# Performance work log

Hardware: AMD Instinct MI355X
Metric: run time of the kernel (lower is better)

The kernel has to match this reference:

```python
import jax, jax.numpy as jnp
import numpy as np

TOPK = 10
NUM_CLASSES = 80
ALPHA = 0.5
BETA = 6.0
EPS = 1e-9
IOU_EPS = 1e-7


def _make_anchors(img=640, strides=(8, 16, 32)):
    pts = []
    for s in strides:
        n = img // s
        ax = (np.arange(n, dtype=np.float32) + 0.5) * s
        gy, gx = np.meshgrid(ax, ax, indexing='ij')
        pts.append(np.stack([gx.ravel(), gy.ravel()], axis=-1))
    return jnp.asarray(np.concatenate(pts, axis=0), dtype=jnp.float32)  # [8400, 2]


def setup_inputs() -> dict:
    key = jax.random.key(0)
    ks = jax.random.split(key, 8)
    bs, ng, nc = 32, 64, NUM_CLASSES
    anc_points = _make_anchors()
    na = anc_points.shape[0]  # 8400
    pd_scores = jax.random.uniform(ks[0], (bs, na, nc), dtype=jnp.float32)
    pwh = jax.random.uniform(ks[1], (bs, na, 2), minval=10.0, maxval=100.0)
    pxy = anc_points[None] + jax.random.normal(ks[2], (bs, na, 2)) * 8.0
    pd_bboxes = jnp.concatenate([pxy - pwh / 2, pxy + pwh / 2], axis=-1)
    gxy = jax.random.uniform(ks[3], (bs, ng, 2), minval=50.0, maxval=590.0)
    gwh = jax.random.uniform(ks[4], (bs, ng, 2), minval=20.0, maxval=200.0)
    gt_bboxes = jnp.clip(jnp.concatenate([gxy - gwh / 2, gxy + gwh / 2], axis=-1), 0.0, 640.0)
    gt_labels = jax.random.randint(ks[5], (bs, ng, 1), 0, nc)
    num_gt = jax.random.randint(ks[6], (bs,), 1, ng + 1)
    mask_gt = (jnp.arange(ng)[None, :] < num_gt[:, None])[..., None]  # bool [bs, ng, 1]
    return {"pd_scores": pd_scores, "pd_bboxes": pd_bboxes, "anc_points": anc_points,
            "gt_labels": gt_labels, "gt_bboxes": gt_bboxes, "mask_gt": mask_gt}


def _iou_xyxy(b1, b2):
    # b1: [bs, na, 1, 4], b2: [bs, 1, ng, 4] -> [bs, na, ng]
    inter_w = jnp.maximum(jnp.minimum(b1[..., 2], b2[..., 2]) - jnp.maximum(b1[..., 0], b2[..., 0]), 0.0)
    inter_h = jnp.maximum(jnp.minimum(b1[..., 3], b2[..., 3]) - jnp.maximum(b1[..., 1], b2[..., 1]), 0.0)
    inter = inter_w * inter_h
    a1 = (b1[..., 2] - b1[..., 0]) * (b1[..., 3] - b1[..., 1])
    a2 = (b2[..., 2] - b2[..., 0]) * (b2[..., 3] - b2[..., 1])
    return inter / (a1 + a2 - inter + IOU_EPS)


def _assign(pd_scores, pd_bboxes, anc_points, gt_labels, gt_bboxes, mask_gt):
    bs, na, nc = pd_scores.shape
    ng = gt_bboxes.shape[1]
    dt = pd_scores.dtype

    # --- candidates whose center lies strictly inside the GT box ---
    lt = gt_bboxes[:, None, :, :2]          # [bs,1,ng,2]
    rb = gt_bboxes[:, None, :, 2:]
    xy = anc_points[None, :, None, :]       # [1,na,1,2]
    deltas = jnp.concatenate([xy - lt, rb - xy], axis=-1)  # [bs,na,ng,4]
    mask_in_gts = deltas.min(axis=-1) > EPS                 # [bs,na,ng]
    valid = mask_gt[..., 0].astype(bool)                    # [bs,ng]
    mask = mask_in_gts & valid[:, None, :]

    # --- alignment metric = score[label]^alpha * iou^beta, zeroed outside mask ---
    labels = gt_labels[..., 0].astype(jnp.int32)            # [bs,ng]
    idx = jnp.broadcast_to(labels[:, None, :], (bs, na, ng))
    gathered = jnp.take_along_axis(pd_scores, idx, axis=2)  # [bs,na,ng]
    bbox_scores = jnp.where(mask, gathered, 0.0)
    overlaps = jnp.where(mask, _iou_xyxy(pd_bboxes[:, :, None, :], gt_bboxes[:, None, :, :]), 0.0)
    safe_scores = jnp.where(mask, gathered, 1.0)  # avoids 0**0.5 grad issues; masked out below
    align_metric = jnp.where(mask, safe_scores ** ALPHA * overlaps ** BETA, 0.0)

    # --- top-k anchors per GT (over anchor dim) ---
    k = min(TOPK, na)
    _, topk_idx = jax.lax.top_k(jnp.swapaxes(align_metric, 1, 2), k)  # [bs,ng,k]
    bidx = jnp.arange(bs)[:, None, None]
    gidx = jnp.arange(ng)[None, :, None]
    in_topk = jnp.zeros((bs, ng, na), dtype=bool).at[bidx, gidx, topk_idx].set(True)
    in_topk = jnp.swapaxes(in_topk, 1, 2) & valid[:, None, :]  # [bs,na,ng]
    mask_pos = (in_topk & mask).astype(dt)

    # --- resolve anchors assigned to multiple GTs by highest IoU ---
    multi = mask_pos.sum(-1, keepdims=True) > 1
    is_max = jax.nn.one_hot(jnp.argmax(overlaps, axis=-1), ng, dtype=dt)
    mask_pos = jnp.where(multi, is_max, mask_pos)
    fg_mask = mask_pos.sum(-1) > 0                  # [bs,na] bool
    target_gt_idx = jnp.argmax(mask_pos, axis=-1)   # [bs,na]

    # --- gather targets ---
    flat_idx = target_gt_idx + jnp.arange(bs)[:, None] * ng
    target_labels = jnp.maximum(gt_labels[..., 0].reshape(-1)[flat_idx], 0)  # [bs,na]
    target_bboxes = gt_bboxes.reshape(-1, 4)[flat_idx]                       # [bs,na,4]
    one_hot = jax.nn.one_hot(target_labels, nc, dtype=dt) * fg_mask[..., None].astype(dt)

    fgf = fg_mask[..., None].astype(dt)
    norm_align = jnp.maximum((align_metric * fgf).max(-1, keepdims=True), EPS)
    norm_overlap = jnp.maximum((overlaps * fgf).max(-1, keepdims=True), EPS)
    t_scores = ((align_metric / norm_align) * (overlaps / norm_overlap) * fgf).max(-1)  # [bs,na]
    target_scores = one_hot * t_scores[..., None]
    return target_labels, target_bboxes, target_scores, fg_mask, target_gt_idx


def reference(pd_scores, pd_bboxes, anc_points, gt_labels, gt_bboxes, mask_gt):
    return _assign(pd_scores, pd_bboxes, anc_points, gt_labels, gt_bboxes, mask_gt)
```

## Files before the change

### kernel.cpp

```cpp
#include <hip/hip_runtime.h>
#include <math.h>

#define NC 80
#define TOPKK 10
#define EPSF 1e-9f
#define IOU_EPSF 1e-7f
#define NA 8400
#define NGMAX 64

typedef float f4nt __attribute__((ext_vector_type(4)));

__device__ __forceinline__ float iou_xyxy(float px0, float py0, float px1, float py1,
                                          float parea,
                                          float gx0, float gy0, float gx1, float gy1,
                                          float garea) {
    float iw = fmaxf(fminf(px1, gx1) - fmaxf(px0, gx0), 0.0f);
    float ih = fmaxf(fminf(py1, gy1) - fmaxf(py0, gy0), 0.0f);
    float inter = iw * ih;
    return inter / (parea + garea - inter + IOU_EPSF);
}

__device__ __forceinline__ float align_metric(float s, float ov) {
    float ov2 = ov * ov;
    return sqrtf(s) * (ov2 * ov2 * ov2);
}

__global__ __launch_bounds__(256) void topk_rect_kernel(
    const float* __restrict__ pd_scores, const float* __restrict__ pd_bboxes,
    const int* __restrict__ gt_labels, const float* __restrict__ gt_bboxes,
    const int* __restrict__ mask_gt,
    unsigned long long* __restrict__ bits, int ng, int total_bg)
{
    int lin = blockIdx.x * 4 + (threadIdx.x >> 6);
    if (lin >= total_bg) return;
    int b = lin / ng;
    int g = lin - b * ng;
    if (mask_gt[b * ng + g] == 0) return;
    int lane = threadIdx.x & 63;

    int lab = gt_labels[b * ng + g];
    float4 gb = ((const float4*)gt_bboxes)[b * ng + g];
    float garea = (gb.z - gb.x) * (gb.w - gb.y);
    const float* __restrict__ srow = pd_scores + ((long)b * NA) * NC + lab;
    const float4* __restrict__ pbb = (const float4*)(pd_bboxes + (long)b * NA * 4);

    const int ls[3] = {8, 16, 32};
    const int ln[3] = {80, 40, 20};
    const int lb[3] = {0, 6400, 8000};
    int jlo[3], ilo[3], rw[3], cnt[3];
    int tot = 0;
#pragma unroll
    for (int l = 0; l < 3; ++l) {
        float s = (float)ls[l];
        int j0 = (int)floorf(gb.x / s - 0.5f) - 1; if (j0 < 0) j0 = 0;
        int j1 = (int)ceilf (gb.z / s - 0.5f) + 1; if (j1 > ln[l] - 1) j1 = ln[l] - 1;
        int i0 = (int)floorf(gb.y / s - 0.5f) - 1; if (i0 < 0) i0 = 0;
        int i1 = (int)ceilf (gb.w / s - 0.5f) + 1; if (i1 > ln[l] - 1) i1 = ln[l] - 1;
        int w = j1 - j0 + 1; if (w < 0) w = 0;
        int h = i1 - i0 + 1; if (h < 0) h = 0;
        jlo[l] = j0; ilo[l] = i0; rw[l] = w; cnt[l] = w * h; tot += cnt[l];
    }

    float lv[TOPKK]; int li[TOPKK];
#pragma unroll
    for (int j = 0; j < TOPKK; ++j) { lv[j] = -1.0f; li[j] = -1; }

    for (int t = lane; t < tot; t += 64) {
        int l = 0, r = t;
        if (r >= cnt[0]) { r -= cnt[0]; l = 1; }
        if (l == 1 && r >= cnt[1]) { r -= cnt[1]; l = 2; }
        int i  = r / rw[l];
        int j  = r - i * rw[l];
        int ii = ilo[l] + i, jj = jlo[l] + j;
        int a  = lb[l] + ii * ln[l] + jj;
        float s  = (float)ls[l];
        float ax = (jj + 0.5f) * s, ay = (ii + 0.5f) * s;
        float d0 = ax - gb.x, d1 = ay - gb.y, d2 = gb.z - ax, d3 = gb.w - ay;
        float dmin = fminf(fminf(d0, d1), fminf(d2, d3));
        if (dmin > EPSF) {
            float4 pb = pbb[a];
            float parea = (pb.z - pb.x) * (pb.w - pb.y);
            float ov = iou_xyxy(pb.x, pb.y, pb.z, pb.w, parea,
                                gb.x, gb.y, gb.z, gb.w, garea);
            float sc = srow[(long)a * NC];
            float v = align_metric(sc, ov);
            if (v > 0.0f && v > lv[TOPKK - 1]) {
                float nv[TOPKK]; int ni[TOPKK];
#pragma unroll
                for (int q = 0; q < TOPKK; ++q) {
                    bool keep = (lv[q] >= v);
                    bool atp  = (q == 0) ? !keep : (!keep && (lv[q - 1] >= v));
                    nv[q] = keep ? lv[q] : (atp ? v : lv[q - 1]);
                    ni[q] = keep ? li[q] : (atp ? a : li[q - 1]);
                }
#pragma unroll
                for (int q = 0; q < TOPKK; ++q) { lv[q] = nv[q]; li[q] = ni[q]; }
            }
        }
    }

    long bbase = (long)b * NA;
    int m = 0;
    for (int it = 0; it < TOPKK; ++it) {
        unsigned long long myk = (lv[0] > 0.0f)
            ? (((unsigned long long)__float_as_uint(lv[0]) << 32)
               | (unsigned)(~(unsigned)li[0]))
            : 0ull;
        unsigned long long k = myk;
#pragma unroll
        for (int off = 32; off > 0; off >>= 1) {
            unsigned long long o = __shfl_xor(k, off, 64);
            k = (o > k) ? o : k;
        }
        if (k == 0ull) break;
        if (myk == k) {
            atomicOr(&bits[bbase + li[0]], 1ull << g);
#pragma unroll
            for (int q = 0; q < TOPKK - 1; ++q) { lv[q] = lv[q + 1]; li[q] = li[q + 1]; }
            lv[TOPKK - 1] = -1.0f; li[TOPKK - 1] = -1;
        }
        m++;
    }

    if (m < TOPKK && lane == 0) {
        int need = TOPKK - m;
        for (int a = 0; need > 0 && a < NA; ++a) {
            int l  = (a < 6400) ? 0 : ((a < 8000) ? 1 : 2);
            int rr = a - lb[l];
            int ii = rr / ln[l];
            int jj = rr - ii * ln[l];
            float s  = (float)ls[l];
            float ax = (jj + 0.5f) * s, ay = (ii + 0.5f) * s;
            float d0 = ax - gb.x, d1 = ay - gb.y, d2 = gb.z - ax, d3 = gb.w - ay;
            float dmin = fminf(fminf(d0, d1), fminf(d2, d3));
            bool positive = false;
            if (dmin > EPSF) {
                float4 pb = pbb[a];
                float parea = (pb.z - pb.x) * (pb.w - pb.y);
                float ov = iou_xyxy(pb.x, pb.y, pb.z, pb.w, parea,
                                    gb.x, gb.y, gb.z, gb.w, garea);
                float sc = srow[(long)a * NC];
                positive = (align_metric(sc, ov) > 0.0f);
            }
            if (!positive) {
                atomicOr(&bits[bbase + a], 1ull << g);
                need--;
            }
        }
    }
}

__global__ __launch_bounds__(256) void assign_scores_kernel(
    const float* __restrict__ pd_scores, const float* __restrict__ pd_bboxes,
    const float* __restrict__ anc, const int* __restrict__ gt_labels,
    const float* __restrict__ gt_bboxes, const int* __restrict__ mask_gt,
    const unsigned long long* __restrict__ bits,
    float* __restrict__ out_labels, float* __restrict__ out_bboxes,
    float* __restrict__ out_scores, float* __restrict__ out_fg,
    float* __restrict__ out_tgt, int ng, int blocksPerB)
{
    __shared__ float4 sgt[NGMAX];
    __shared__ float  sarea[NGMAX];
    __shared__ int    slab[NGMAX];
    __shared__ int    svalid[NGMAX];
    __shared__ int    plab[256];
    __shared__ float  pt[256];

    int b  = blockIdx.x / blocksPerB;
    int a0 = (blockIdx.x - b * blocksPerB) * 256;
    int a  = a0 + threadIdx.x;

    for (int g = threadIdx.x; g < ng; g += 256) {
        float4 gb = ((const float4*)gt_bboxes)[b * ng + g];
        sgt[g] = gb;
        sarea[g] = (gb.z - gb.x) * (gb.w - gb.y);
        slab[g] = gt_labels[b * ng + g];
        svalid[g] = mask_gt[b * ng + g];
    }
    __syncthreads();

    bool alive = (a < NA);
    int labi0 = slab[0] < 0 ? 0 : slab[0];
    int labi = labi0; float t = 0.0f;

    if (alive) {
        long ba = (long)b * NA + a;
        unsigned long long w = bits[ba];
        if (w == 0ull) {
            out_labels[ba] = (float)labi0;
            ((float4*)out_bboxes)[ba] = sgt[0];
            out_fg[ba]  = 0.0f;
            out_tgt[ba] = 0.0f;
        } else {
            float ax = anc[a * 2 + 0];
            float ay = anc[a * 2 + 1];
            float4 pb = ((const float4*)pd_bboxes)[ba];
            float parea = (pb.z - pb.x) * (pb.w - pb.y);
            const float* __restrict__ srow = pd_scores + ba * NC;

            int cnt = 0, pos_g = 0;
            float best_ov = 0.0f; int best_g = 0;
            float m_align = 0.0f, m_ov = 0.0f, t_raw = 0.0f;

            for (int g = 0; g < ng; ++g) {
                if (svalid[g] == 0) break;
                float4 gb = sgt[g];
                float d0 = ax - gb.x, d1 = ay - gb.y, d2 = gb.z - ax, d3 = gb.w - ay;
                float dmin = fminf(fminf(d0, d1), fminf(d2, d3));
                bool mask = (dmin > EPSF);
                float ov = 0.0f, al = 0.0f;
                if (mask) {
                    ov = iou_xyxy(pb.x, pb.y, pb.z, pb.w, parea,
                                  gb.x, gb.y, gb.z, gb.w, sarea[g]);
                    float s = srow[slab[g]];
                    al = align_metric(s, ov);
                }
                bool pos = mask && ((w >> g) & 1ull);
                if (pos) { if (cnt == 0) pos_g = g; cnt++; }
                if (ov > best_ov) { best_ov = ov; best_g = g; }
                m_align = fmaxf(m_align, al);
                m_ov    = fmaxf(m_ov, ov);
                t_raw   = fmaxf(t_raw, al * ov);
            }

            int fg  = (cnt > 0) ? 1 : 0;
            int tgt = (cnt > 1) ? best_g : ((cnt == 1) ? pos_g : 0);

            labi = slab[tgt]; if (labi < 0) labi = 0;
            out_labels[ba] = (float)labi;
            ((float4*)out_bboxes)[ba] = sgt[tgt];
            out_fg[ba]  = (float)fg;
            out_tgt[ba] = (float)tgt;

            if (fg) {
                float na_ = fmaxf(m_align, EPSF);
                float no_ = fmaxf(m_ov, EPSF);
                t = (t_raw / na_) / no_;
            }
        }
    }

    plab[threadIdx.x] = labi;
    pt[threadIdx.x]   = t;
    __syncthreads();

    int cnt_rows = NA - a0; if (cnt_rows > 256) cnt_rows = 256;
    int tot4 = cnt_rows * (NC / 4);
    f4nt* __restrict__ oslab = (f4nt*)(out_scores + ((long)b * NA + a0) * NC);
    for (int i = threadIdx.x; i < tot4; i += 256) {
        int al = i / (NC / 4);
        int cg = (i - al * (NC / 4)) * 4;
        int lab = plab[al];
        float tv = pt[al];
        f4nt o;
        o.x = (cg     == lab) ? tv : 0.0f;
        o.y = (cg + 1 == lab) ? tv : 0.0f;
        o.z = (cg + 2 == lab) ? tv : 0.0f;
        o.w = (cg + 3 == lab) ? tv : 0.0f;
        __builtin_nontemporal_store(o, &oslab[i]);
    }
}

extern "C" void kernel_launch(void* const* d_in, const int* in_sizes, int n_in,
                              void* d_out, int out_size, void* d_ws, size_t ws_size,
                              hipStream_t stream) {
    const float* pd_scores = (const float*)d_in[0];
    const float* pd_bboxes = (const float*)d_in[1];
    const float* anc       = (const float*)d_in[2];
    const int*   gt_labels = (const int*)d_in[3];
    const float* gt_bboxes = (const float*)d_in[4];
    const int*   mask_gt   = (const int*)d_in[5];

    int na = in_sizes[2] / 2;
    int bs = in_sizes[0] / (na * NC);
    int ng = in_sizes[3] / bs;

    long nBA = (long)bs * na;
    float* out        = (float*)d_out;
    float* out_labels = out;
    float* out_bboxes = out + nBA;
    float* out_scores = out + nBA * 5;
    float* out_fg     = out + nBA * 85;
    float* out_tgt    = out + nBA * 86;

    unsigned long long* bits = (unsigned long long*)d_ws;

    hipMemsetAsync(d_ws, 0, nBA * sizeof(unsigned long long), stream);

    int total_bg = bs * ng;
    int nblk = (total_bg + 3) / 4;
    topk_rect_kernel<<<nblk, 256, 0, stream>>>(
        pd_scores, pd_bboxes, gt_labels, gt_bboxes, mask_gt, bits, ng, total_bg);

    int bpb = (na + 255) / 256;
    assign_scores_kernel<<<bs * bpb, 256, 0, stream>>>(
        pd_scores, pd_bboxes, anc, gt_labels, gt_bboxes, mask_gt, bits,
        out_labels, out_bboxes, out_scores, out_fg, out_tgt, ng, bpb);
}
```

Baseline: 200.3 us.

## Replace global candidate bitmask with per-gt top-k index lists built in shared memory

The top-k kernel now writes each gt's selected anchor indices to a compact list instead of atomically OR-ing bits into a per-anchor global bitmask. The assign kernel rebuilds each block's bitmask in shared memory by scanning the batch's index list. This removes the workspace memset and the global atomics. In exchange, every assign block rescans all ng*10 entries for its batch and uses shared-memory atomics.

```diff
diff --git a/kernel.cpp b/kernel.cpp
--- a/kernel.cpp
+++ b/kernel.cpp
@@ -29,14 +29,19 @@
     const float* __restrict__ pd_scores, const float* __restrict__ pd_bboxes,
     const int* __restrict__ gt_labels, const float* __restrict__ gt_bboxes,
     const int* __restrict__ mask_gt,
-    unsigned long long* __restrict__ bits, int ng, int total_bg)
+    int* __restrict__ idx_out, int ng, int total_bg)
 {
     int lin = blockIdx.x * 4 + (threadIdx.x >> 6);
     if (lin >= total_bg) return;
     int b = lin / ng;
     int g = lin - b * ng;
-    if (mask_gt[b * ng + g] == 0) return;
     int lane = threadIdx.x & 63;
+    int* __restrict__ slot = idx_out + (long)lin * TOPKK;
+
+    if (mask_gt[b * ng + g] == 0) {
+        if (lane < TOPKK) slot[lane] = -1;
+        return;
+    }
 
     int lab = gt_labels[b * ng + g];
     float4 gb = ((const float4*)gt_bboxes)[b * ng + g];
@@ -99,7 +104,6 @@
         }
     }
 
-    long bbase = (long)b * NA;
     int m = 0;
     for (int it = 0; it < TOPKK; ++it) {
         unsigned long long myk = (lv[0] > 0.0f)
@@ -114,7 +118,7 @@
         }
         if (k == 0ull) break;
         if (myk == k) {
-            atomicOr(&bits[bbase + li[0]], 1ull << g);
+            slot[it] = li[0];
 #pragma unroll
             for (int q = 0; q < TOPKK - 1; ++q) { lv[q] = lv[q + 1]; li[q] = li[q + 1]; }
             lv[TOPKK - 1] = -1.0f; li[TOPKK - 1] = -1;
@@ -123,8 +127,8 @@
     }
 
     if (m < TOPKK && lane == 0) {
-        int need = TOPKK - m;
-        for (int a = 0; need > 0 && a < NA; ++a) {
+        int p = m;
+        for (int a = 0; p < TOPKK && a < NA; ++a) {
             int l  = (a < 6400) ? 0 : ((a < 8000) ? 1 : 2);
             int rr = a - lb[l];
             int ii = rr / ln[l];
@@ -142,10 +146,7 @@
                 float sc = srow[(long)a * NC];
                 positive = (align_metric(sc, ov) > 0.0f);
             }
-            if (!positive) {
-                atomicOr(&bits[bbase + a], 1ull << g);
-                need--;
-            }
+            if (!positive) slot[p++] = a;
         }
     }
 }
@@ -154,7 +155,7 @@
     const float* __restrict__ pd_scores, const float* __restrict__ pd_bboxes,
     const float* __restrict__ anc, const int* __restrict__ gt_labels,
     const float* __restrict__ gt_bboxes, const int* __restrict__ mask_gt,
-    const unsigned long long* __restrict__ bits,
+    const int* __restrict__ idx_in,
     float* __restrict__ out_labels, float* __restrict__ out_bboxes,
     float* __restrict__ out_scores, float* __restrict__ out_fg,
     float* __restrict__ out_tgt, int ng, int blocksPerB)
@@ -163,6 +164,7 @@
     __shared__ float  sarea[NGMAX];
     __shared__ int    slab[NGMAX];
     __shared__ int    svalid[NGMAX];
+    __shared__ unsigned long long smask[256];
     __shared__ int    plab[256];
     __shared__ float  pt[256];
 
@@ -170,6 +172,7 @@
     int a0 = (blockIdx.x - b * blocksPerB) * 256;
     int a  = a0 + threadIdx.x;
 
+    smask[threadIdx.x] = 0ull;
     for (int g = threadIdx.x; g < ng; g += 256) {
         float4 gb = ((const float4*)gt_bboxes)[b * ng + g];
         sgt[g] = gb;
@@ -179,13 +182,26 @@
     }
     __syncthreads();
 
+    {
+        int nent = ng * TOPKK;
+        const int* lst = idx_in + (long)b * nent;
+        for (int i = threadIdx.x; i < nent; i += 256) {
+            int aa = lst[i];
+            unsigned off = (unsigned)(aa - a0);
+            if (aa >= 0 && off < 256u) {
+                atomicOr(&smask[off], 1ull << (i / TOPKK));
+            }
+        }
+    }
+    __syncthreads();
+
     bool alive = (a < NA);
     int labi0 = slab[0] < 0 ? 0 : slab[0];
     int labi = labi0; float t = 0.0f;
 
     if (alive) {
         long ba = (long)b * NA + a;
-        unsigned long long w = bits[ba];
+        unsigned long long w = smask[threadIdx.x];
         if (w == 0ull) {
             out_labels[ba] = (float)labi0;
             ((float4*)out_bboxes)[ba] = sgt[0];
@@ -283,17 +299,15 @@
     float* out_fg     = out + nBA * 85;
     float* out_tgt    = out + nBA * 86;
 
-    unsigned long long* bits = (unsigned long long*)d_ws;
-
-    hipMemsetAsync(d_ws, 0, nBA * sizeof(unsigned long long), stream);
+    int* idx = (int*)d_ws;
 
     int total_bg = bs * ng;
     int nblk = (total_bg + 3) / 4;
     topk_rect_kernel<<<nblk, 256, 0, stream>>>(
-        pd_scores, pd_bboxes, gt_labels, gt_bboxes, mask_gt, bits, ng, total_bg);
+        pd_scores, pd_bboxes, gt_labels, gt_bboxes, mask_gt, idx, ng, total_bg);
 
     int bpb = (na + 255) / 256;
     assign_scores_kernel<<<bs * bpb, 256, 0, stream>>>(
-        pd_scores, pd_bboxes, anc, gt_labels, gt_bboxes, mask_gt, bits,
+        pd_scores, pd_bboxes, anc, gt_labels, gt_bboxes, mask_gt, idx,
         out_labels, out_bboxes, out_scores, out_fg, out_tgt, ng, bpb);
 }
```

After: 197.4 us. No clear change (-1.5%).
